# Kernel optimization log

Measured on AMD Instinct MI355X. Metric: run time of the kernel, lower is better.

Reference implementation:

```python
import jax, jax.numpy as jnp
import numpy as np

B, E, D, H, A = 65536, 16, 256, 64, 18  # batch, n_subpolicies, emb_dim, hidden, n_actions


def setup_inputs() -> dict:
    key = jax.random.key(0)
    ks = jax.random.split(key, 16)
    s = lambda k, sh: jax.random.normal(k, sh, dtype=jnp.float32) * 0.05
    return dict(
        obs=s(ks[0], (B, D)),
        h=s(ks[1], (B, D)),
        c=s(ks[2], (B, D)),
        idxs=jax.random.randint(ks[3], (B,), 0, E, dtype=jnp.int32),
        # Observer: LSTMCell(D, D) params (torch layout: [4D, D] with i,f,g,o gate order)
        W_ih=s(ks[4], (4 * D, D)), W_hh=s(ks[5], (4 * D, D)),
        b_ih=s(ks[6], (4 * D,)), b_hh=s(ks[7], (4 * D,)),
        # Stacked SubPolicy actor params: Linear(D,64)-Tanh-Linear(64,A)
        Wa1=s(ks[8], (E, D, H)), ba1=s(ks[9], (E, H)),
        Wa2=s(ks[10], (E, H, A)), ba2=s(ks[11], (E, A)),
        # Stacked SubPolicy critic params: Linear(D,64)-Tanh-Linear(64,1)
        Wc1=s(ks[12], (E, D, H)), bc1=s(ks[13], (E, H)),
        Wc2=s(ks[14], (E, H, 1)), bc2=s(ks[15], (E, 1)),
    )


def reference(obs, h, c, idxs, W_ih, W_hh, b_ih, b_hh,
              Wa1, ba1, Wa2, ba2, Wc1, bc1, Wc2, bc2):
    # ---- Observer: single LSTMCell step ----
    gates = obs @ W_ih.T + b_ih + h @ W_hh.T + b_hh          # [B, 4D]
    gi, gf, gg, go = jnp.split(gates, 4, axis=1)
    i = jax.nn.sigmoid(gi); f = jax.nn.sigmoid(gf); o = jax.nn.sigmoid(go)
    c_new = f * c + i * jnp.tanh(gg)                          # [B, D]
    h_new = o * jnp.tanh(c_new)                               # [B, D]

    # ---- Expert dispatch: evaluate all tiny subpolicy MLPs, select per sample ----
    # (mathematically identical to the per-sample routing loop in forward_sub)
    ha = jnp.tanh(jnp.einsum('bd,edh->beh', h_new, Wa1) + ba1)        # [B, E, H]
    logits_all = jnp.einsum('beh,eha->bea', ha, Wa2) + ba2            # [B, E, A]
    hc = jnp.tanh(jnp.einsum('bd,edh->beh', h_new, Wc1) + bc1)        # [B, E, H]
    vals_all = (jnp.einsum('beh,eho->beo', hc, Wc2) + bc2)[..., 0]    # [B, E]

    b = jnp.arange(h_new.shape[0])
    logits = logits_all[b, idxs]                                       # [B, A]
    values = vals_all[b, idxs]                                         # [B]
    return (h_new, c_new, logits, values)
```

## Files before the change

### kernel.cpp

```cpp
#include <hip/hip_runtime.h>
#include <hip/hip_bf16.h>
#include <math.h>

#define NB 65536
#define ND 256
#define NE 16
#define NH 64
#define NA 18

typedef __bf16 bf16;
typedef __bf16 bf16x4 __attribute__((ext_vector_type(4)));
typedef __bf16 bf16x8 __attribute__((ext_vector_type(8)));
typedef float  f32x4  __attribute__((ext_vector_type(4)));

#define OFF_WCAT 0u
#define OFF_BCAT 1048576u
#define OFF_PW1  1052672u
#define OFF_B1   2101248u
#define OFF_CUR  2109440u
#define OFF_PERM 2109504u

__device__ __forceinline__ float sigm_(float x) {
    return 1.f / (1.f + __expf(-x));
}
__device__ __forceinline__ float tanh_(float x) {
    float cl = fminf(fmaxf(x, -15.f), 15.f);
    float e = __expf(2.f * cl);
    return (e - 1.f) / (e + 1.f);
}

__global__ void k_prep1(const float* __restrict__ W_ih, const float* __restrict__ W_hh,
                        const float* __restrict__ b_ih, const float* __restrict__ b_hh,
                        char* __restrict__ ws) {
    int t = blockIdx.x * 256 + threadIdx.x;
    bf16* Wcat = (bf16*)(ws + OFF_WCAT);
    int kc = t & 63, col = t >> 6;
    int k = kc * 8;
    const float* src = (k < 256) ? (W_ih + (size_t)col * 256 + k)
                                 : (W_hh + (size_t)col * 256 + (k - 256));
    float4 v0 = *(const float4*)(src);
    float4 v1 = *(const float4*)(src + 4);
    bf16x8 o;
    o[0] = (bf16)v0.x; o[1] = (bf16)v0.y; o[2] = (bf16)v0.z; o[3] = (bf16)v0.w;
    o[4] = (bf16)v1.x; o[5] = (bf16)v1.y; o[6] = (bf16)v1.z; o[7] = (bf16)v1.w;
    *(bf16x8*)(Wcat + ((size_t)kc * 1024 + col) * 8) = o;
    if (t < 1024) ((float*)(ws + OFF_BCAT))[t] = b_ih[t] + b_hh[t];
    if (t < 16)   ((int*)(ws + OFF_CUR))[t] = t * 65536;
}

__global__ void k_prep2(const float* __restrict__ Wa1, const float* __restrict__ Wc1,
                        const float* __restrict__ ba1, const float* __restrict__ bc1,
                        char* __restrict__ ws) {
    int t = blockIdx.x * 256 + threadIdx.x;
    bf16* PW1 = (bf16*)(ws + OFF_PW1);
    int col = t & 127, kc = (t >> 7) & 31, e = t >> 12;
    bf16x8 o;
#pragma unroll
    for (int j = 0; j < 8; ++j) {
        int k = kc * 8 + j;
        float v = (col < 64) ? Wa1[((size_t)e * 256 + k) * 64 + col]
                             : Wc1[((size_t)e * 256 + k) * 64 + (col - 64)];
        o[j] = (bf16)v;
    }
    *(bf16x8*)(PW1 + (((size_t)e * 32 + kc) * 128 + col) * 8) = o;
    if (t < 2048) {
        int e2 = t >> 7, c = t & 127;
        ((float*)(ws + OFF_B1))[t] = (c < 64) ? ba1[e2 * 64 + c] : bc1[e2 * 64 + (c - 64)];
    }
}

__global__ void k_scatter(const int* __restrict__ idxs, char* __restrict__ ws) {
    __shared__ int lh[16], lbase[16];
    int t = threadIdx.x;
    int i = blockIdx.x * 256 + t;
    if (t < 16) lh[t] = 0;
    __syncthreads();
    int e = idxs[i];
    int r = atomicAdd(&lh[e], 1);
    __syncthreads();
    int* cur = (int*)(ws + OFF_CUR);
    if (t < 16) lbase[t] = atomicAdd(&cur[t], lh[t]);
    __syncthreads();
    ((int*)(ws + OFF_PERM))[lbase[e] + r] = i;
}

__global__ __launch_bounds__(1024) void k_lstm(
    const float* __restrict__ obs, const float* __restrict__ hin,
    const float* __restrict__ cin, const float* __restrict__ bcat,
    const bf16* __restrict__ Wcat,
    float* __restrict__ hout, float* __restrict__ cout) {
    __shared__ alignas(16) bf16 Alds[8 * 64 * 8];
    const int tid  = threadIdx.x;
    const int wave = tid >> 6, lane = tid & 63;
    const int lr = lane & 15, lk = lane >> 4;
    const int row0 = blockIdx.x * 64;
    const int srow = tid >> 4, sf4 = tid & 15;

    f32x4 acc[4][4];
#pragma unroll
    for (int m = 0; m < 4; ++m)
#pragma unroll
        for (int g = 0; g < 4; ++g)
#pragma unroll
            for (int r = 0; r < 4; ++r) acc[m][g][r] = 0.f;

    for (int ks = 0; ks < 8; ++ks) {
        int k0 = ks * 64;
        const float* sp = (k0 < 256)
            ? (obs + (size_t)(row0 + srow) * 256 + k0 + sf4 * 4)
            : (hin + (size_t)(row0 + srow) * 256 + (k0 - 256) + sf4 * 4);
        float4 v = *(const float4*)sp;
        bf16x4 pw;
        pw[0] = (bf16)v.x; pw[1] = (bf16)v.y; pw[2] = (bf16)v.z; pw[3] = (bf16)v.w;
        *(bf16x4*)(Alds + (((sf4 >> 1) * 64 + srow) * 8) + (sf4 & 1) * 4) = pw;
        __syncthreads();

        int kcg0 = ks * 8;
#pragma unroll
        for (int kf = 0; kf < 2; ++kf) {
            bf16x8 a[4], bb[4];
#pragma unroll
            for (int m = 0; m < 4; ++m)
                a[m] = *(const bf16x8*)(Alds + (((kf * 4 + lk) * 64) + (m * 16 + lr)) * 8);
#pragma unroll
            for (int g = 0; g < 4; ++g) {
                int col = g * 256 + wave * 16 + lr;
                int kc  = kcg0 + kf * 4 + lk;
                bb[g] = *(const bf16x8*)(Wcat + ((size_t)kc * 1024 + col) * 8);
            }
#pragma unroll
            for (int m = 0; m < 4; ++m)
#pragma unroll
                for (int g = 0; g < 4; ++g)
                    acc[m][g] = __builtin_amdgcn_mfma_f32_16x16x32_bf16(a[m], bb[g], acc[m][g], 0, 0, 0);
        }
        __syncthreads();
    }

    int col = wave * 16 + lr;
    float bi = bcat[col], bf_ = bcat[256 + col], bg = bcat[512 + col], bo = bcat[768 + col];
#pragma unroll
    for (int m = 0; m < 4; ++m) {
#pragma unroll
        for (int r = 0; r < 4; ++r) {
            int row = row0 + m * 16 + lk * 4 + r;
            float gi = acc[m][0][r] + bi;
            float gf = acc[m][1][r] + bf_;
            float gg = acc[m][2][r] + bg;
            float go = acc[m][3][r] + bo;
            float iv = sigm_(gi), fv = sigm_(gf), gv = tanh_(gg), ov = sigm_(go);
            float co = cin[(size_t)row * 256 + col];
            float cn = fv * co + iv * gv;
            float hn = ov * tanh_(cn);
            cout[(size_t)row * 256 + col] = cn;
            hout[(size_t)row * 256 + col] = hn;
        }
    }
}

__global__ __launch_bounds__(256) void k_expert(
    const float* __restrict__ Wa2, const float* __restrict__ ba2,
    const float* __restrict__ Wc2, const float* __restrict__ bc2,
    char* __restrict__ ws, const float* __restrict__ hsrc,
    float* __restrict__ lout, float* __restrict__ vout) {
    const int e = blockIdx.y;
    const int* cur = (const int*)(ws + OFF_CUR);
    int cnt = cur[e] - e * 65536;
    int r0 = blockIdx.x * 64;
    if (r0 >= cnt) return;
    int nr = min(64, cnt - r0);
    const int* permE = (const int*)(ws + OFF_PERM) + (size_t)e * 65536 + r0;

    __shared__ int rows_s[64];
    __shared__ alignas(16) char smem[128 * 66 * 4];
    bf16*  Alds = (bf16*)smem;
    float* haF  = (float*)smem;

    int t = threadIdx.x;
    if (t < 64) rows_s[t] = permE[(t < nr) ? t : 0];
    __syncthreads();

    {
        int rowi = t >> 2, q = t & 3;
        const float* hp = hsrc + (size_t)rows_s[rowi] * 256;
#pragma unroll
        for (int s = 0; s < 8; ++s) {
            int kc = s * 4 + q;
            float4 v0 = *(const float4*)(hp + kc * 8);
            float4 v1 = *(const float4*)(hp + kc * 8 + 4);
            bf16x8 o;
            o[0] = (bf16)v0.x; o[1] = (bf16)v0.y; o[2] = (bf16)v0.z; o[3] = (bf16)v0.w;
            o[4] = (bf16)v1.x; o[5] = (bf16)v1.y; o[6] = (bf16)v1.z; o[7] = (bf16)v1.w;
            *(bf16x8*)(Alds + ((size_t)kc * 64 + rowi) * 8) = o;
        }
    }
    __syncthreads();

    const bf16* PW1 = (const bf16*)(ws + OFF_PW1) + (size_t)e * 32 * 128 * 8;
    const float* b1 = (const float*)(ws + OFF_B1) + e * 128;
    int wave = t >> 6, lane = t & 63, lr = lane & 15, lk = lane >> 4;

    f32x4 acc[4][2];
#pragma unroll
    for (int m = 0; m < 4; ++m)
#pragma unroll
        for (int n = 0; n < 2; ++n)
#pragma unroll
            for (int r = 0; r < 4; ++r) acc[m][n][r] = 0.f;

#pragma unroll
    for (int kf = 0; kf < 8; ++kf) {
        bf16x8 a[4], bb[2];
#pragma unroll
        for (int m = 0; m < 4; ++m)
            a[m] = *(const bf16x8*)(Alds + (((kf * 4 + lk) * 64) + (m * 16 + lr)) * 8);
#pragma unroll
        for (int n = 0; n < 2; ++n) {
            int colh = wave * 32 + n * 16 + lr;
            int kc = kf * 4 + lk;
            bb[n] = *(const bf16x8*)(PW1 + ((size_t)kc * 128 + colh) * 8);
        }
#pragma unroll
        for (int m = 0; m < 4; ++m)
#pragma unroll
            for (int n = 0; n < 2; ++n)
                acc[m][n] = __builtin_amdgcn_mfma_f32_16x16x32_bf16(a[m], bb[n], acc[m][n], 0, 0, 0);
    }
    __syncthreads();

#pragma unroll
    for (int m = 0; m < 4; ++m)
#pragma unroll
        for (int n = 0; n < 2; ++n) {
            int colh = wave * 32 + n * 16 + lr;
            float bbv = b1[colh];
#pragma unroll
            for (int r = 0; r < 4; ++r) {
                int row = m * 16 + lk * 4 + r;
                haF[colh * 66 + row] = tanh_(acc[m][n][r] + bbv);
            }
        }
    __syncthreads();

    int row = t & 63;
    int grow = rows_s[row];
    bool valid = row < nr;
#pragma unroll
    for (int p = 0; p < 5; ++p) {
        int aI = p * 4 + (t >> 6);
        if (aI < NA) {
            float s = ba2[e * NA + aI];
            for (int hh = 0; hh < 64; ++hh)
                s += haF[hh * 66 + row] * Wa2[((size_t)e * 64 + hh) * NA + aI];
            if (valid) lout[(size_t)grow * NA + aI] = s;
        }
    }
    if (t < 64) {
        float s = bc2[e];
        for (int hh = 0; hh < 64; ++hh)
            s += haF[(64 + hh) * 66 + row] * Wc2[e * 64 + hh];
        if (valid) vout[grow] = s;
    }
}

extern "C" void kernel_launch(void* const* d_in, const int* in_sizes, int n_in,
                              void* d_out, int out_size, void* d_ws, size_t ws_size,
                              hipStream_t stream) {
    const float* obs  = (const float*)d_in[0];
    const float* h    = (const float*)d_in[1];
    const float* c    = (const float*)d_in[2];
    const int*   idxs = (const int*)d_in[3];
    const float* W_ih = (const float*)d_in[4];
    const float* W_hh = (const float*)d_in[5];
    const float* b_ih = (const float*)d_in[6];
    const float* b_hh = (const float*)d_in[7];
    const float* Wa1  = (const float*)d_in[8];
    const float* ba1  = (const float*)d_in[9];
    const float* Wa2  = (const float*)d_in[10];
    const float* ba2  = (const float*)d_in[11];
    const float* Wc1  = (const float*)d_in[12];
    const float* bc1  = (const float*)d_in[13];
    const float* Wc2  = (const float*)d_in[14];
    const float* bc2  = (const float*)d_in[15];

    float* out  = (float*)d_out;
    float* hout = out;
    float* cout = out + (size_t)NB * ND;
    float* lout = out + (size_t)2 * NB * ND;
    float* vout = lout + (size_t)NB * NA;
    char* ws = (char*)d_ws;

    k_prep1<<<dim3(256), dim3(256), 0, stream>>>(W_ih, W_hh, b_ih, b_hh, ws);
    k_prep2<<<dim3(256), dim3(256), 0, stream>>>(Wa1, Wc1, ba1, bc1, ws);
    k_scatter<<<dim3(256), dim3(256), 0, stream>>>(idxs, ws);
    k_lstm<<<dim3(1024), dim3(1024), 0, stream>>>(
        obs, h, c, (const float*)(ws + OFF_BCAT), (const bf16*)(ws + OFF_WCAT), hout, cout);
    k_expert<<<dim3(1024, 16), dim3(256), 0, stream>>>(
        Wa2, ba2, Wc2, bc2, ws, hout, lout, vout);
}
```

Before: 221.6 us.

## Double-buffer LSTM GEMM LDS tiles with swizzle and split columns across blocks

The LSTM gate GEMM kernel now uses 512-thread blocks, with each block handling half of the hidden columns, so 2048 blocks are launched instead of 1024. The A-tile staging is double-buffered in LDS with register prefetch of the next k-slice. This overlaps global loads with MFMA work and removes one barrier per iteration. Rows are XOR-swizzled to avoid LDS bank conflicts. The cost is that the obs/h rows are now loaded and converted twice, once per column half.

```diff
diff --git a/kernel.cpp b/kernel.cpp
--- a/kernel.cpp
+++ b/kernel.cpp
@@ -84,17 +84,33 @@
     ((int*)(ws + OFF_PERM))[lbase[e] + r] = i;
 }
 
-__global__ __launch_bounds__(1024) void k_lstm(
+__global__ __launch_bounds__(512, 4) void k_lstm(
     const float* __restrict__ obs, const float* __restrict__ hin,
     const float* __restrict__ cin, const float* __restrict__ bcat,
     const bf16* __restrict__ Wcat,
     float* __restrict__ hout, float* __restrict__ cout) {
-    __shared__ alignas(16) bf16 Alds[8 * 64 * 8];
+    __shared__ alignas(16) char Asmem[2][8192];
     const int tid  = threadIdx.x;
     const int wave = tid >> 6, lane = tid & 63;
     const int lr = lane & 15, lk = lane >> 4;
-    const int row0 = blockIdx.x * 64;
-    const int srow = tid >> 4, sf4 = tid & 15;
+    const int rb = blockIdx.x & 1023, chalf = blockIdx.x >> 10;
+    const int row0 = rb * 64;
+    const int srow = tid >> 3, sf = tid & 7;
+    const int colc = chalf * 128 + wave * 16 + lr;
+
+    const int wbyte = sf * 1024 + ((srow ^ sf) * 16);
+    int rbo[2][4];
+#pragma unroll
+    for (int kf = 0; kf < 2; ++kf)
+#pragma unroll
+        for (int m = 0; m < 4; ++m) {
+            int kc = kf * 4 + lk, R = m * 16 + lr;
+            rbo[kf][m] = kc * 1024 + ((R ^ kc) * 16);
+        }
+
+    const float* pObs = obs + (size_t)(row0 + srow) * 256 + sf * 8;
+    const float* pH   = hin + (size_t)(row0 + srow) * 256 + sf * 8;
+    const bf16*  pB   = Wcat + ((size_t)lk * 1024 + colc) * 8;
 
     f32x4 acc[4][4];
 #pragma unroll
@@ -104,41 +120,55 @@
 #pragma unroll
             for (int r = 0; r < 4; ++r) acc[m][g][r] = 0.f;
 
+    {
+        float4 v0 = *(const float4*)pObs;
+        float4 v1 = *(const float4*)(pObs + 4);
+        bf16x8 o;
+        o[0] = (bf16)v0.x; o[1] = (bf16)v0.y; o[2] = (bf16)v0.z; o[3] = (bf16)v0.w;
+        o[4] = (bf16)v1.x; o[5] = (bf16)v1.y; o[6] = (bf16)v1.z; o[7] = (bf16)v1.w;
+        *(bf16x8*)(&Asmem[0][wbyte]) = o;
+    }
+    __syncthreads();
+
+#pragma unroll
     for (int ks = 0; ks < 8; ++ks) {
-        int k0 = ks * 64;
-        const float* sp = (k0 < 256)
-            ? (obs + (size_t)(row0 + srow) * 256 + k0 + sf4 * 4)
-            : (hin + (size_t)(row0 + srow) * 256 + (k0 - 256) + sf4 * 4);
-        float4 v = *(const float4*)sp;
-        bf16x4 pw;
-        pw[0] = (bf16)v.x; pw[1] = (bf16)v.y; pw[2] = (bf16)v.z; pw[3] = (bf16)v.w;
-        *(bf16x4*)(Alds + (((sf4 >> 1) * 64 + srow) * 8) + (sf4 & 1) * 4) = pw;
-        __syncthreads();
-
-        int kcg0 = ks * 8;
+        const int cur = ks & 1;
+        float4 n0, n1;
+        if (ks < 7) {
+            const float* sp = (ks < 3) ? (pObs + (ks + 1) * 64) : (pH + (ks - 3) * 64);
+            n0 = *(const float4*)sp;
+            n1 = *(const float4*)(sp + 4);
+        }
+        const char* Ab = Asmem[cur];
 #pragma unroll
         for (int kf = 0; kf < 2; ++kf) {
-            bf16x8 a[4], bb[4];
+            bf16x8 a[4];
 #pragma unroll
             for (int m = 0; m < 4; ++m)
-                a[m] = *(const bf16x8*)(Alds + (((kf * 4 + lk) * 64) + (m * 16 + lr)) * 8);
-#pragma unroll
-            for (int g = 0; g < 4; ++g) {
-                int col = g * 256 + wave * 16 + lr;
-                int kc  = kcg0 + kf * 4 + lk;
-                bb[g] = *(const bf16x8*)(Wcat + ((size_t)kc * 1024 + col) * 8);
+                a[m] = *(const bf16x8*)(Ab + rbo[kf][m]);
+            const bf16* pBk = pB + (size_t)(ks * 8 + kf * 4) * 1024 * 8;
+            bf16x8 b0 = *(const bf16x8*)(pBk);
+            bf16x8 b1 = *(const bf16x8*)(pBk + 256 * 8);
+            bf16x8 b2 = *(const bf16x8*)(pBk + 512 * 8);
+            bf16x8 b3 = *(const bf16x8*)(pBk + 768 * 8);
+#pragma unroll
+            for (int m = 0; m < 4; ++m) {
+                acc[m][0] = __builtin_amdgcn_mfma_f32_16x16x32_bf16(a[m], b0, acc[m][0], 0, 0, 0);
+                acc[m][1] = __builtin_amdgcn_mfma_f32_16x16x32_bf16(a[m], b1, acc[m][1], 0, 0, 0);
+                acc[m][2] = __builtin_amdgcn_mfma_f32_16x16x32_bf16(a[m], b2, acc[m][2], 0, 0, 0);
+                acc[m][3] = __builtin_amdgcn_mfma_f32_16x16x32_bf16(a[m], b3, acc[m][3], 0, 0, 0);
             }
-#pragma unroll
-            for (int m = 0; m < 4; ++m)
-#pragma unroll
-                for (int g = 0; g < 4; ++g)
-                    acc[m][g] = __builtin_amdgcn_mfma_f32_16x16x32_bf16(a[m], bb[g], acc[m][g], 0, 0, 0);
-        }
-        __syncthreads();
-    }
-
-    int col = wave * 16 + lr;
-    float bi = bcat[col], bf_ = bcat[256 + col], bg = bcat[512 + col], bo = bcat[768 + col];
+        }
+        if (ks < 7) {
+            bf16x8 o;
+            o[0] = (bf16)n0.x; o[1] = (bf16)n0.y; o[2] = (bf16)n0.z; o[3] = (bf16)n0.w;
+            o[4] = (bf16)n1.x; o[5] = (bf16)n1.y; o[6] = (bf16)n1.z; o[7] = (bf16)n1.w;
+            *(bf16x8*)(&Asmem[cur ^ 1][wbyte]) = o;
+            __syncthreads();
+        }
+    }
+
+    float bi = bcat[colc], bf_ = bcat[256 + colc], bg = bcat[512 + colc], bo = bcat[768 + colc];
 #pragma unroll
     for (int m = 0; m < 4; ++m) {
 #pragma unroll
@@ -149,11 +179,11 @@
             float gg = acc[m][2][r] + bg;
             float go = acc[m][3][r] + bo;
             float iv = sigm_(gi), fv = sigm_(gf), gv = tanh_(gg), ov = sigm_(go);
-            float co = cin[(size_t)row * 256 + col];
+            float co = cin[(size_t)row * 256 + colc];
             float cn = fv * co + iv * gv;
             float hn = ov * tanh_(cn);
-            cout[(size_t)row * 256 + col] = cn;
-            hout[(size_t)row * 256 + col] = hn;
+            cout[(size_t)row * 256 + colc] = cn;
+            hout[(size_t)row * 256 + colc] = hn;
         }
     }
 }
@@ -293,7 +323,7 @@
     k_prep1<<<dim3(256), dim3(256), 0, stream>>>(W_ih, W_hh, b_ih, b_hh, ws);
     k_prep2<<<dim3(256), dim3(256), 0, stream>>>(Wa1, Wc1, ba1, bc1, ws);
     k_scatter<<<dim3(256), dim3(256), 0, stream>>>(idxs, ws);
-    k_lstm<<<dim3(1024), dim3(1024), 0, stream>>>(
+    k_lstm<<<dim3(2048), dim3(512), 0, stream>>>(
         obs, h, c, (const float*)(ws + OFF_BCAT), (const bf16*)(ws + OFF_WCAT), hout, cout);
     k_expert<<<dim3(1024, 16), dim3(256), 0, stream>>>(
         Wa2, ba2, Wc2, bc2, ws, hout, lout, vout);
```

Result: faster. 193.9 us (-12.5%).
